# Kernel tuning notes

Hardware: AMD Instinct MI355X
Metric: run time of the kernel (lower is better)

## Reference

```python
import jax, jax.numpy as jnp
import numpy as np

B, T, I, E, H = 512, 1024, 32, 32, 256  # batch, seq, input, time-enc, hidden


def setup_inputs() -> dict:
    key = jax.random.key(0)
    ks = jax.random.split(key, 10)
    s = 0.05
    return {
        "X": jax.random.normal(ks[0], (B, T, I), dtype=jnp.float32),
        "encoded_timestamps": jax.random.normal(ks[1], (B, T, E), dtype=jnp.float32),
        "mask": jax.random.randint(ks[2], (B, T), 0, 2).astype(bool),
        # GRU layer 0: input = I + E
        "w_ih0": jax.random.normal(ks[3], (3 * H, I + E), dtype=jnp.float32) * s,
        "w_hh0": jax.random.normal(ks[4], (3 * H, H), dtype=jnp.float32) * s,
        "b_ih0": jnp.zeros((3 * H,), jnp.float32),
        "b_hh0": jnp.zeros((3 * H,), jnp.float32),
        # GRU layer 1: input = H
        "w_ih1": jax.random.normal(ks[5], (3 * H, H), dtype=jnp.float32) * s,
        "w_hh1": jax.random.normal(ks[6], (3 * H, H), dtype=jnp.float32) * s,
        "b_ih1": jnp.zeros((3 * H,), jnp.float32),
        "b_hh1": jnp.zeros((3 * H,), jnp.float32),
        # readout Linear(H -> I)
        "w_out": jax.random.normal(ks[7], (I, H), dtype=jnp.float32) * s,
        "b_out": jnp.zeros((I,), jnp.float32),
    }


def _gru_cell(x, h, w_ih, w_hh, b_ih, b_hh):
    # torch GRU cell semantics (gate order r, z, n)
    gi = x @ w_ih.T + b_ih
    gh = h @ w_hh.T + b_hh
    i_r, i_z, i_n = jnp.split(gi, 3, axis=-1)
    h_r, h_z, h_n = jnp.split(gh, 3, axis=-1)
    r = jax.nn.sigmoid(i_r + h_r)
    z = jax.nn.sigmoid(i_z + h_z)
    n = jnp.tanh(i_n + r * h_n)
    return (1.0 - z) * n + z * h


def reference(X, encoded_timestamps, mask,
              w_ih0, w_hh0, b_ih0, b_hh0,
              w_ih1, w_hh1, b_ih1, b_hh1,
              w_out, b_out):
    b, t, _ = X.shape
    hdim = w_hh0.shape[1]
    tm1 = t - 1

    def step(carry, xs):
        h0, h1, y = carry
        x_t, e_t, m_t, first = xs          # x_t [B,I], e_t [B,E], m_t [B], first scalar bool
        keep = m_t | first
        inp = jnp.concatenate([jnp.where(keep[:, None], x_t, y), e_t], axis=-1)
        h0 = _gru_cell(inp, h0, w_ih0, w_hh0, b_ih0, b_hh0)
        h1 = _gru_cell(h0, h1, w_ih1, w_hh1, b_ih1, b_hh1)
        y = h1 @ w_out.T + b_out
        return (h0, h1, y), y

    init = (jnp.zeros((b, hdim), X.dtype),
            jnp.zeros((b, hdim), X.dtype),
            jnp.zeros((b, X.shape[2]), X.dtype))
    xs = (jnp.swapaxes(X[:, :tm1], 0, 1),
          jnp.swapaxes(encoded_timestamps[:, 1:], 0, 1),
          jnp.swapaxes(mask[:, :tm1], 0, 1),
          jnp.arange(tm1) == 0)
    (h0, h1, _), outs = jax.lax.scan(step, init, xs)
    output_sequence = jnp.swapaxes(outs, 0, 1)  # [B, T-1, I]
    return output_sequence, h1  # h1 == h_t[-1]
```

## Files before the change

kernel.cpp:

```cpp
#include <hip/hip_runtime.h>
#include <stdint.h>
#include <stddef.h>

typedef unsigned short u16;
typedef unsigned int u32;
typedef unsigned long long u64;
typedef __attribute__((ext_vector_type(8))) short short8;
typedef __attribute__((ext_vector_type(4))) float f32x4;
typedef __attribute__((ext_vector_type(2))) float f32x2;

#define B_    512
#define T_    1024
#define TM1_  1023
#define I_    32
#define E_    32
#define H_    256
#define GSZ   16
#define NGRP  16
#define NTH   512
#define HBUF  (B_ * H_)
#define OUTY_STRIDE (TM1_ * I_)
#define OUTH_BASE ((size_t)B_ * TM1_ * I_)
#define FLAG_STRIDE 16

__device__ __forceinline__ u16 f2bf(float f) {
  union { float f; unsigned int i; } c;
  c.f = f;
  unsigned int x = c.i;
  x += 0x7FFFu + ((x >> 16) & 1u);
  return (u16)(x >> 16);
}
__device__ __forceinline__ short8 ld8bf(const float* p) {
  short8 rv;
#pragma unroll
  for (int j = 0; j < 8; ++j) rv[j] = (short)f2bf(p[j]);
  return rv;
}
__device__ __forceinline__ float sigm(float x) { return 1.f / (1.f + __expf(-x)); }
__device__ __forceinline__ float tanh_fast(float x) {
  x = fminf(15.f, fmaxf(-15.f, x));
  float e = __expf(2.f * x);
  return (e - 1.f) / (e + 1.f);
}
__device__ __forceinline__ u64 ldq_cp(const u64* p) { return *(volatile const u64*)p; }
__device__ __forceinline__ void stw_cp(u32* p, u32 v) { *(volatile u32*)p = v; }

__global__ __launch_bounds__(NTH, 2)
void arrnn_persistent(
    const float* __restrict__ X, const float* __restrict__ ENC, const int* __restrict__ MASK,
    const float* __restrict__ wih0, const float* __restrict__ whh0,
    const float* __restrict__ bih0, const float* __restrict__ bhh0,
    const float* __restrict__ wih1, const float* __restrict__ whh1,
    const float* __restrict__ bih1, const float* __restrict__ bhh1,
    const float* __restrict__ wout, const float* __restrict__ bout,
    float* __restrict__ out, u16* __restrict__ h0g, u16* __restrict__ h1g,
    int* __restrict__ flags)
{
  __shared__ __align__(16) u16 sH0buf[32 * 264];
  __shared__ __align__(16) u16 sH1buf[32 * 264];
  __shared__ __align__(16) u16 sXE[32 * 72];
  __shared__ float sGates[4 * 32 * 20];
  __shared__ float sH0loc[512];
  __shared__ float sH1loc[512];
  __shared__ float sY[32 * 36];
  __shared__ int   sMk[32];

  const int tid  = threadIdx.x;
  const int w    = tid >> 6;
  const int lane = tid & 63;
  const int quad = lane >> 4;
  const int l15  = lane & 15;
  const int g    = blockIdx.x >> 4;
  const int r    = blockIdx.x & 15;
  const int hs   = r << 4;
  const int row0 = g << 5;
  const int mt   = w & 1;
  const int gt   = w >> 1;
  const int crow = tid >> 4;
  const int cdim = tid & 15;

  short8 zero8 = {0, 0, 0, 0, 0, 0, 0, 0};

  const int grow = ((gt == 1) ? 256 : (gt >= 2 ? 512 : 0)) + hs + l15;

  short8 wfA[10];
#pragma unroll
  for (int kk = 0; kk < 10; ++kk) {
    const int k = kk * 32 + quad * 8;
    const float* p;
    bool v;
    if (gt <= 1)      { v = true;     p = (k < 64) ? (wih0 + grow * 64 + k)
                                                   : (whh0 + grow * 256 + (k - 64)); }
    else if (gt == 2) { v = (kk < 2); p = wih0 + grow * 64 + (v ? k : 0); }
    else              { v = (kk < 8); p = whh0 + grow * 256 + (v ? k : 0); }
    wfA[kk] = v ? ld8bf(p) : zero8;
  }

  short8 wfB[16];
#pragma unroll
  for (int kk = 0; kk < 16; ++kk) {
    const int k = kk * 32 + quad * 8;
    const float* p;
    bool v;
    if (gt <= 1)      { v = true;     p = (k < 256) ? (wih1 + grow * 256 + k)
                                                    : (whh1 + grow * 256 + (k - 256)); }
    else if (gt == 2) { v = (kk < 8); p = wih1 + grow * 256 + (v ? k : 0); }
    else              { v = (kk < 8); p = whh1 + grow * 256 + (v ? k : 0); }
    wfB[kk] = v ? ld8bf(p) : zero8;
  }

  const int yout = ((w >> 1) & 1) * 16 + l15;
  short8 wfY[8];
  if (w < 4) {
#pragma unroll
    for (int kk = 0; kk < 8; ++kk)
      wfY[kk] = ld8bf(wout + yout * 256 + kk * 32 + quad * 8);
  } else {
#pragma unroll
    for (int kk = 0; kk < 8; ++kk) wfY[kk] = zero8;
  }
  const float boutv = (w < 4) ? bout[yout] : 0.f;

  const int bd = hs + cdim;
  const float b0r  = bih0[bd]       + bhh0[bd];
  const float b0z  = bih0[256 + bd] + bhh0[256 + bd];
  const float b0ni = bih0[512 + bd];
  const float b0nh = bhh0[512 + bd];
  const float b1r  = bih1[bd]       + bhh1[bd];
  const float b1z  = bih1[256 + bd] + bhh1[256 + bd];
  const float b1ni = bih1[512 + bd];
  const float b1nh = bhh1[512 + bd];

  for (int i = tid; i < 4224; i += NTH) {
    ((u32*)sH0buf)[i] = 0u;
    ((u32*)sH1buf)[i] = 0u;
  }
  sH0loc[tid] = 0.f;
  sH1loc[tid] = 0.f;
  __syncthreads();

  const u64* h0q = (const u64*)h0g;
  const u64* h1q = (const u64*)h1g;
  u32* h0u = (u32*)h0g;
  u32* h1u = (u32*)h1g;

  int* fH0g  = flags + g * GSZ * FLAG_STRIDE;
  int* fH1g  = flags + NGRP * GSZ * FLAG_STRIDE + g * GSZ * FLAG_STRIDE;
  int* fH0own = fH0g + r * FLAG_STRIDE;
  int* fH1own = fH1g + r * FLAG_STRIDE;
  int alive = 1;

#define WAIT_FLAGS(basep, tgt)                                                   \
  do {                                                                           \
    int ok = 1;                                                                  \
    if (alive && lane < GSZ) {                                                   \
      const int* fp = (basep) + lane * FLAG_STRIDE;                              \
      int it = 0;                                                                \
      while (__hip_atomic_load(fp, __ATOMIC_RELAXED,                             \
                               __HIP_MEMORY_SCOPE_SYSTEM) < (tgt)) {             \
        __builtin_amdgcn_s_sleep(1);                                             \
        if (++it > (1 << 16)) { ok = 0; break; }                                 \
      }                                                                          \
    }                                                                            \
    if (__ballot(ok == 0) != 0ull) alive = 0;                                    \
  } while (0)

#define POST_FLAG(fp, val)                                                       \
  do {                                                                           \
    if (tid == 0) {                                                              \
      __builtin_amdgcn_s_waitcnt(0);                                             \
      __hip_atomic_store((fp), (val), __ATOMIC_RELAXED,                          \
                         __HIP_MEMORY_SCOPE_SYSTEM);                             \
    }                                                                            \
  } while (0)

  const int b = row0 + crow;
  const int arow = mt * 16 + l15;

  for (int t = 0; t < 1024; ++t) {
    const int par = t & 1;

    int mk = 1;
    if (t < 1023) {
      f32x2 xld = *(const f32x2*)(X   + ((size_t)b * T_ + t)     * I_ + 2 * cdim);
      f32x2 eld = *(const f32x2*)(ENC + ((size_t)b * T_ + t + 1) * E_ + 2 * cdim);
      if (t > 0) mk = (MASK[b * T_ + t] != 0);
      u16* A = sXE + crow * 72;
      const int c2 = 2 * cdim;
      if (mk) { A[c2] = f2bf(xld.x); A[c2 + 1] = f2bf(xld.y); }
      A[32 + c2] = f2bf(eld.x); A[32 + c2 + 1] = f2bf(eld.y);
      if (cdim == 0) sMk[crow] = mk;
    }

    f32x4 accA = {0.f, 0.f, 0.f, 0.f};
    if (t < 1023) {
      if (gt <= 1) {
        const u16* ah = sH0buf + arow * 264 + quad * 8;
#pragma unroll
        for (int kk = 2; kk < 10; ++kk) {
          short8 af = *(const short8*)(ah + (kk - 2) * 32);
          accA = __builtin_amdgcn_mfma_f32_16x16x32_bf16(af, wfA[kk], accA, 0, 0, 0);
        }
      } else if (gt == 3) {
        const u16* ah = sH0buf + arow * 264 + quad * 8;
#pragma unroll
        for (int kk = 0; kk < 8; ++kk) {
          short8 af = *(const short8*)(ah + kk * 32);
          accA = __builtin_amdgcn_mfma_f32_16x16x32_bf16(af, wfA[kk], accA, 0, 0, 0);
        }
      }
    }

    if (t > 0) {
      if (w == 0) WAIT_FLAGS(fH1g, t);
      __syncthreads();
      const u64* hq = h1q + (size_t)par * 32768 + (size_t)b * 64 + cdim * 4;
      u64 q0 = ldq_cp(hq), q1 = ldq_cp(hq + 1), q2 = ldq_cp(hq + 2), q3 = ldq_cp(hq + 3);
      union { u64 q[2]; short8 s; } u0, u1;
      u0.q[0] = q0; u0.q[1] = q1; u1.q[0] = q2; u1.q[1] = q3;
      *(short8*)(sH1buf + crow * 264 + cdim * 16)     = u0.s;
      *(short8*)(sH1buf + crow * 264 + cdim * 16 + 8) = u1.s;
    }
    __syncthreads();

    if (t > 0 && w < 4) {
      const u16* ap = sH1buf + (mt * 16 + l15) * 264 + quad * 8;
      f32x4 acc = {0.f, 0.f, 0.f, 0.f};
#pragma unroll
      for (int kk = 0; kk < 8; ++kk) {
        short8 af = *(const short8*)(ap + kk * 32);
        acc = __builtin_amdgcn_mfma_f32_16x16x32_bf16(af, wfY[kk], acc, 0, 0, 0);
      }
#pragma unroll
      for (int rg = 0; rg < 4; ++rg) {
        const int row = mt * 16 + quad * 4 + rg;
        const float yv = acc[rg] + boutv;
        sY[row * 36 + yout] = yv;
        if (t < 1023 && !sMk[row]) sXE[row * 72 + yout] = f2bf(yv);
      }
    }
    __syncthreads();

    if (t > 0 && tid < 64) {
      const int lr = r * 2 + (tid >> 5);
      const int lc = tid & 31;
      out[(size_t)(row0 + lr) * OUTY_STRIDE + (size_t)(t - 1) * I_ + lc] =
          sY[lr * 36 + lc];
    }
    if (t == 1023) break;

    if (gt <= 2) {
      const u16* axe = sXE + arow * 72 + quad * 8;
#pragma unroll
      for (int kk = 0; kk < 2; ++kk) {
        short8 af = *(const short8*)(axe + kk * 32);
        accA = __builtin_amdgcn_mfma_f32_16x16x32_bf16(af, wfA[kk], accA, 0, 0, 0);
      }
    }
#pragma unroll
    for (int rg = 0; rg < 4; ++rg)
      sGates[(gt * 32 + mt * 16 + quad * 4 + rg) * 20 + l15] = accA[rg];
    __syncthreads();

    {
      const float gr = sGates[(0 * 32 + crow) * 20 + cdim] + b0r;
      const float gz = sGates[(1 * 32 + crow) * 20 + cdim] + b0z;
      const float gi = sGates[(2 * 32 + crow) * 20 + cdim] + b0ni;
      const float gh = sGates[(3 * 32 + crow) * 20 + cdim] + b0nh;
      const float rr = sigm(gr);
      const float zz = sigm(gz);
      const float nn = tanh_fast(gi + rr * gh);
      const float hv = (1.f - zz) * nn + zz * sH0loc[tid];
      sH0loc[tid] = hv;
      const float hp = __shfl_xor(hv, 1, 64);
      if (!(tid & 1)) {
        u32 pk = (u32)f2bf(hv) | ((u32)f2bf(hp) << 16);
        stw_cp(h0u + (size_t)(par ^ 1) * 65536 + (size_t)b * 128 + ((hs + cdim) >> 1), pk);
      }
    }
    __syncthreads();
    POST_FLAG(fH0own, t + 1);

    f32x4 accB = {0.f, 0.f, 0.f, 0.f};
    if (gt <= 1) {
      const u16* a1 = sH1buf + arow * 264 + quad * 8;
#pragma unroll
      for (int kk = 0; kk < 8; ++kk) {
        short8 af = *(const short8*)(a1 + kk * 32);
        accB = __builtin_amdgcn_mfma_f32_16x16x32_bf16(af, wfB[kk + 8], accB, 0, 0, 0);
      }
    } else if (gt == 3) {
      const u16* a1 = sH1buf + arow * 264 + quad * 8;
#pragma unroll
      for (int kk = 0; kk < 8; ++kk) {
        short8 af = *(const short8*)(a1 + kk * 32);
        accB = __builtin_amdgcn_mfma_f32_16x16x32_bf16(af, wfB[kk], accB, 0, 0, 0);
      }
    }

    if (w == 0) WAIT_FLAGS(fH0g, t + 1);
    __syncthreads();
    {
      const u64* hq = h0q + (size_t)(par ^ 1) * 32768 + (size_t)b * 64 + cdim * 4;
      u64 q0 = ldq_cp(hq), q1 = ldq_cp(hq + 1), q2 = ldq_cp(hq + 2), q3 = ldq_cp(hq + 3);
      union { u64 q[2]; short8 s; } u0, u1;
      u0.q[0] = q0; u0.q[1] = q1; u1.q[0] = q2; u1.q[1] = q3;
      *(short8*)(sH0buf + crow * 264 + cdim * 16)     = u0.s;
      *(short8*)(sH0buf + crow * 264 + cdim * 16 + 8) = u1.s;
    }
    __syncthreads();

    if (gt <= 2) {
      const u16* a0 = sH0buf + arow * 264 + quad * 8;
#pragma unroll
      for (int kk = 0; kk < 8; ++kk) {
        short8 af = *(const short8*)(a0 + kk * 32);
        accB = __builtin_amdgcn_mfma_f32_16x16x32_bf16(af, wfB[kk], accB, 0, 0, 0);
      }
    }
#pragma unroll
    for (int rg = 0; rg < 4; ++rg)
      sGates[(gt * 32 + mt * 16 + quad * 4 + rg) * 20 + l15] = accB[rg];
    __syncthreads();

    {
      const float gr = sGates[(0 * 32 + crow) * 20 + cdim] + b1r;
      const float gz = sGates[(1 * 32 + crow) * 20 + cdim] + b1z;
      const float gi = sGates[(2 * 32 + crow) * 20 + cdim] + b1ni;
      const float gh = sGates[(3 * 32 + crow) * 20 + cdim] + b1nh;
      const float rr = sigm(gr);
      const float zz = sigm(gz);
      const float nn = tanh_fast(gi + rr * gh);
      const float hv = (1.f - zz) * nn + zz * sH1loc[tid];
      sH1loc[tid] = hv;
      const float hp = __shfl_xor(hv, 1, 64);
      if (!(tid & 1)) {
        u32 pk = (u32)f2bf(hv) | ((u32)f2bf(hp) << 16);
        stw_cp(h1u + (size_t)(par ^ 1) * 65536 + (size_t)b * 128 + ((hs + cdim) >> 1), pk);
      }
    }
    __syncthreads();
    POST_FLAG(fH1own, t + 1);
  }

  out[OUTH_BASE + (size_t)b * H_ + hs + cdim] = sH1loc[tid];
#undef WAIT_FLAGS
#undef POST_FLAG
}

extern "C" void kernel_launch(void* const* d_in, const int* in_sizes, int n_in,
                              void* d_out, int out_size, void* d_ws, size_t ws_size,
                              hipStream_t stream) {
  (void)in_sizes; (void)n_in; (void)out_size; (void)ws_size;
  const float* X    = (const float*)d_in[0];
  const float* ENC  = (const float*)d_in[1];
  const int*   MASK = (const int*)d_in[2];
  const float* wih0 = (const float*)d_in[3];
  const float* whh0 = (const float*)d_in[4];
  const float* bih0 = (const float*)d_in[5];
  const float* bhh0 = (const float*)d_in[6];
  const float* wih1 = (const float*)d_in[7];
  const float* whh1 = (const float*)d_in[8];
  const float* bih1 = (const float*)d_in[9];
  const float* bhh1 = (const float*)d_in[10];
  const float* wout = (const float*)d_in[11];
  const float* bout = (const float*)d_in[12];
  float* out = (float*)d_out;

  char* ws = (char*)d_ws;
  u16* h0g = (u16*)ws;
  u16* h1g = (u16*)(ws + 2 * (size_t)HBUF * 2);
  int* flags = (int*)(ws + 4 * (size_t)HBUF * 2);

  hipMemsetAsync(flags, 0, 2 * NGRP * GSZ * FLAG_STRIDE * sizeof(int), stream);
  arrnn_persistent<<<dim3(NGRP * GSZ), dim3(NTH), 0, stream>>>(
      X, ENC, MASK, wih0, whh0, bih0, bhh0, wih1, whh1, bih1, bhh1,
      wout, bout, out, h0g, h1g, flags);
}
```

Measured before the change: 6.313 ms.

## Replace flag barriers with tagged mailbox words and regroup into 8-block groups

Hidden-state exchange between blocks now uses a mailbox in which each 32-bit word carries a bf16 value and the step tag. Consumers spin directly on the data words instead of waiting on separate per-block flags, which removes the flag store/load round trip and some block-wide barriers. Groups change from 16 blocks of 32 rows to 8 blocks of 16 rows with a 32-wide hidden slice per block, so fewer peers take part in each group exchange. In exchange, mailbox traffic doubles because each value uses 32 bits, and every thread now spins on global memory.

Result: faster. 5.383 ms (-14.7%).

```diff
diff --git a/kernel.cpp b/kernel.cpp
--- a/kernel.cpp
+++ b/kernel.cpp
@@ -15,13 +15,12 @@
 #define I_    32
 #define E_    32
 #define H_    256
-#define GSZ   16
-#define NGRP  16
+#define GSZ   8
+#define NGRP  32
 #define NTH   512
-#define HBUF  (B_ * H_)
+#define MBOX_PAR (B_ * H_)
 #define OUTY_STRIDE (TM1_ * I_)
 #define OUTH_BASE ((size_t)B_ * TM1_ * I_)
-#define FLAG_STRIDE 16
 
 __device__ __forceinline__ u16 f2bf(float f) {
   union { float f; unsigned int i; } c;
@@ -53,35 +52,35 @@
     const float* __restrict__ wih1, const float* __restrict__ whh1,
     const float* __restrict__ bih1, const float* __restrict__ bhh1,
     const float* __restrict__ wout, const float* __restrict__ bout,
-    float* __restrict__ out, u16* __restrict__ h0g, u16* __restrict__ h1g,
-    int* __restrict__ flags)
+    float* __restrict__ out, u32* __restrict__ h0m, u32* __restrict__ h1m)
 {
-  __shared__ __align__(16) u16 sH0buf[32 * 264];
-  __shared__ __align__(16) u16 sH1buf[32 * 264];
-  __shared__ __align__(16) u16 sXE[32 * 72];
-  __shared__ float sGates[4 * 32 * 20];
+  __shared__ __align__(16) u16 sH0buf[16 * 264];
+  __shared__ __align__(16) u16 sH1buf[16 * 264];
+  __shared__ __align__(16) u16 sXE[16 * 72];
+  __shared__ float sGates[8 * 16 * 20];
   __shared__ float sH0loc[512];
   __shared__ float sH1loc[512];
-  __shared__ float sY[32 * 36];
-  __shared__ int   sMk[32];
+  __shared__ float sY[16 * 36];
+  __shared__ int   sMk[16];
 
   const int tid  = threadIdx.x;
   const int w    = tid >> 6;
   const int lane = tid & 63;
   const int quad = lane >> 4;
   const int l15  = lane & 15;
-  const int g    = blockIdx.x >> 4;
-  const int r    = blockIdx.x & 15;
-  const int hs   = r << 4;
-  const int row0 = g << 5;
-  const int mt   = w & 1;
+  const int g    = blockIdx.x >> 3;
+  const int r    = blockIdx.x & 7;
+  const int hs   = r << 5;
+  const int row0 = g << 4;
   const int gt   = w >> 1;
-  const int crow = tid >> 4;
-  const int cdim = tid & 15;
+  const int nt   = w & 1;
+  const int crow = tid >> 5;
+  const int c32  = tid & 31;
 
   short8 zero8 = {0, 0, 0, 0, 0, 0, 0, 0};
 
-  const int grow = ((gt == 1) ? 256 : (gt >= 2 ? 512 : 0)) + hs + l15;
+  const int gateofs = (gt == 1) ? 256 : (gt >= 2 ? 512 : 0);
+  const int grow = gateofs + hs + (nt << 4) + l15;
 
   short8 wfA[10];
 #pragma unroll
@@ -109,19 +108,19 @@
     wfB[kk] = v ? ld8bf(p) : zero8;
   }
 
-  const int yout = ((w >> 1) & 1) * 16 + l15;
+  const int ycol = (w << 4) + l15;
   short8 wfY[8];
-  if (w < 4) {
+  if (w < 2) {
 #pragma unroll
     for (int kk = 0; kk < 8; ++kk)
-      wfY[kk] = ld8bf(wout + yout * 256 + kk * 32 + quad * 8);
+      wfY[kk] = ld8bf(wout + ycol * 256 + kk * 32 + quad * 8);
   } else {
 #pragma unroll
     for (int kk = 0; kk < 8; ++kk) wfY[kk] = zero8;
   }
-  const float boutv = (w < 4) ? bout[yout] : 0.f;
-
-  const int bd = hs + cdim;
+  const float boutv = (w < 2) ? bout[ycol] : 0.f;
+
+  const int bd = hs + c32;
   const float b0r  = bih0[bd]       + bhh0[bd];
   const float b0z  = bih0[256 + bd] + bhh0[256 + bd];
   const float b0ni = bih0[512 + bd];
@@ -131,7 +130,7 @@
   const float b1ni = bih1[512 + bd];
   const float b1nh = bhh1[512 + bd];
 
-  for (int i = tid; i < 4224; i += NTH) {
+  for (int i = tid; i < 2112; i += NTH) {
     ((u32*)sH0buf)[i] = 0u;
     ((u32*)sH1buf)[i] = 0u;
   }
@@ -139,213 +138,170 @@
   sH1loc[tid] = 0.f;
   __syncthreads();
 
-  const u64* h0q = (const u64*)h0g;
-  const u64* h1q = (const u64*)h1g;
-  u32* h0u = (u32*)h0g;
-  u32* h1u = (u32*)h1g;
-
-  int* fH0g  = flags + g * GSZ * FLAG_STRIDE;
-  int* fH1g  = flags + NGRP * GSZ * FLAG_STRIDE + g * GSZ * FLAG_STRIDE;
-  int* fH0own = fH0g + r * FLAG_STRIDE;
-  int* fH1own = fH1g + r * FLAG_STRIDE;
   int alive = 1;
-
-#define WAIT_FLAGS(basep, tgt)                                                   \
+  const int b = row0 + crow;
+
+#define SPIN_STAGE(mboxu32, expTag, dstbuf)                                      \
   do {                                                                           \
-    int ok = 1;                                                                  \
-    if (alive && lane < GSZ) {                                                   \
-      const int* fp = (basep) + lane * FLAG_STRIDE;                              \
-      int it = 0;                                                                \
-      while (__hip_atomic_load(fp, __ATOMIC_RELAXED,                             \
-                               __HIP_MEMORY_SCOPE_SYSTEM) < (tgt)) {             \
-        __builtin_amdgcn_s_sleep(1);                                             \
-        if (++it > (1 << 16)) { ok = 0; break; }                                 \
-      }                                                                          \
+    const u64* qp = (const u64*)(mboxu32) + (size_t)b * 128 + c32 * 4;           \
+    const u64 tagp = (u64)(u32)(expTag) | ((u64)(u32)(expTag) << 32);            \
+    u64 q0, q1, q2, q3;                                                          \
+    int it = 0;                                                                  \
+    for (;;) {                                                                   \
+      q0 = ldq_cp(qp); q1 = ldq_cp(qp + 1); q2 = ldq_cp(qp + 2); q3 = ldq_cp(qp + 3); \
+      u64 dd = ((q0 ^ tagp) | (q1 ^ tagp) | (q2 ^ tagp) | (q3 ^ tagp))           \
+               & 0x0000FFFF0000FFFFull;                                          \
+      if (dd == 0 || !alive) break;                                              \
+      if (++it > (1 << 16)) { alive = 0; break; }                                \
     }                                                                            \
-    if (__ballot(ok == 0) != 0ull) alive = 0;                                    \
+    short8 sv;                                                                   \
+    sv[0] = (short)(u16)(q0 >> 16); sv[1] = (short)(u16)(q0 >> 48);              \
+    sv[2] = (short)(u16)(q1 >> 16); sv[3] = (short)(u16)(q1 >> 48);              \
+    sv[4] = (short)(u16)(q2 >> 16); sv[5] = (short)(u16)(q2 >> 48);              \
+    sv[6] = (short)(u16)(q3 >> 16); sv[7] = (short)(u16)(q3 >> 48);              \
+    *(short8*)((dstbuf) + crow * 264 + c32 * 8) = sv;                            \
   } while (0)
-
-#define POST_FLAG(fp, val)                                                       \
-  do {                                                                           \
-    if (tid == 0) {                                                              \
-      __builtin_amdgcn_s_waitcnt(0);                                             \
-      __hip_atomic_store((fp), (val), __ATOMIC_RELAXED,                          \
-                         __HIP_MEMORY_SCOPE_SYSTEM);                             \
-    }                                                                            \
-  } while (0)
-
-  const int b = row0 + crow;
-  const int arow = mt * 16 + l15;
 
   for (int t = 0; t < 1024; ++t) {
     const int par = t & 1;
 
     int mk = 1;
     if (t < 1023) {
-      f32x2 xld = *(const f32x2*)(X   + ((size_t)b * T_ + t)     * I_ + 2 * cdim);
-      f32x2 eld = *(const f32x2*)(ENC + ((size_t)b * T_ + t + 1) * E_ + 2 * cdim);
-      if (t > 0) mk = (MASK[b * T_ + t] != 0);
-      u16* A = sXE + crow * 72;
-      const int c2 = 2 * cdim;
-      if (mk) { A[c2] = f2bf(xld.x); A[c2 + 1] = f2bf(xld.y); }
-      A[32 + c2] = f2bf(eld.x); A[32 + c2 + 1] = f2bf(eld.y);
-      if (cdim == 0) sMk[crow] = mk;
+      if (c32 < 16) {
+        if (t > 0) mk = (MASK[b * T_ + t] != 0);
+        f32x2 xld = *(const f32x2*)(X + ((size_t)b * T_ + t) * I_ + 2 * c32);
+        if (mk) { sXE[crow * 72 + 2 * c32] = f2bf(xld.x);
+                  sXE[crow * 72 + 2 * c32 + 1] = f2bf(xld.y); }
+        if (c32 == 0) sMk[crow] = mk;
+      } else {
+        const int c2 = c32 - 16;
+        f32x2 eld = *(const f32x2*)(ENC + ((size_t)b * T_ + t + 1) * E_ + 2 * c2);
+        sXE[crow * 72 + 32 + 2 * c2] = f2bf(eld.x);
+        sXE[crow * 72 + 32 + 2 * c2 + 1] = f2bf(eld.y);
+      }
     }
 
     f32x4 accA = {0.f, 0.f, 0.f, 0.f};
     if (t < 1023) {
+      const u16* ah = sH0buf + l15 * 264 + quad * 8;
       if (gt <= 1) {
-        const u16* ah = sH0buf + arow * 264 + quad * 8;
-#pragma unroll
-        for (int kk = 2; kk < 10; ++kk) {
-          short8 af = *(const short8*)(ah + (kk - 2) * 32);
-          accA = __builtin_amdgcn_mfma_f32_16x16x32_bf16(af, wfA[kk], accA, 0, 0, 0);
-        }
+#pragma unroll
+        for (int kk = 2; kk < 10; ++kk)
+          accA = __builtin_amdgcn_mfma_f32_16x16x32_bf16(
+              *(const short8*)(ah + (kk - 2) * 32), wfA[kk], accA, 0, 0, 0);
       } else if (gt == 3) {
-        const u16* ah = sH0buf + arow * 264 + quad * 8;
-#pragma unroll
-        for (int kk = 0; kk < 8; ++kk) {
-          short8 af = *(const short8*)(ah + kk * 32);
-          accA = __builtin_amdgcn_mfma_f32_16x16x32_bf16(af, wfA[kk], accA, 0, 0, 0);
-        }
+#pragma unroll
+        for (int kk = 0; kk < 8; ++kk)
+          accA = __builtin_amdgcn_mfma_f32_16x16x32_bf16(
+              *(const short8*)(ah + kk * 32), wfA[kk], accA, 0, 0, 0);
       }
     }
 
+    if (t > 0) SPIN_STAGE(h1m + (size_t)par * MBOX_PAR, t, sH1buf);
+    __syncthreads();
+
+    if (t > 0 && w < 2) {
+      const u16* ap = sH1buf + l15 * 264 + quad * 8;
+      f32x4 acc = {0.f, 0.f, 0.f, 0.f};
+#pragma unroll
+      for (int kk = 0; kk < 8; ++kk)
+        acc = __builtin_amdgcn_mfma_f32_16x16x32_bf16(
+            *(const short8*)(ap + kk * 32), wfY[kk], acc, 0, 0, 0);
+#pragma unroll
+      for (int rg = 0; rg < 4; ++rg)
+        sY[(quad * 4 + rg) * 36 + ycol] = acc[rg] + boutv;
+    }
+    __syncthreads();
+
     if (t > 0) {
-      if (w == 0) WAIT_FLAGS(fH1g, t);
-      __syncthreads();
-      const u64* hq = h1q + (size_t)par * 32768 + (size_t)b * 64 + cdim * 4;
-      u64 q0 = ldq_cp(hq), q1 = ldq_cp(hq + 1), q2 = ldq_cp(hq + 2), q3 = ldq_cp(hq + 3);
-      union { u64 q[2]; short8 s; } u0, u1;
-      u0.q[0] = q0; u0.q[1] = q1; u1.q[0] = q2; u1.q[1] = q3;
-      *(short8*)(sH1buf + crow * 264 + cdim * 16)     = u0.s;
-      *(short8*)(sH1buf + crow * 264 + cdim * 16 + 8) = u1.s;
-    }
-    __syncthreads();
-
-    if (t > 0 && w < 4) {
-      const u16* ap = sH1buf + (mt * 16 + l15) * 264 + quad * 8;
-      f32x4 acc = {0.f, 0.f, 0.f, 0.f};
-#pragma unroll
-      for (int kk = 0; kk < 8; ++kk) {
-        short8 af = *(const short8*)(ap + kk * 32);
-        acc = __builtin_amdgcn_mfma_f32_16x16x32_bf16(af, wfY[kk], acc, 0, 0, 0);
+      if (tid < 64) {
+        const int lr = (r << 1) + (tid >> 5);
+        const int lc = tid & 31;
+        out[(size_t)(row0 + lr) * OUTY_STRIDE + (size_t)(t - 1) * I_ + lc] =
+            sY[lr * 36 + lc];
       }
-#pragma unroll
-      for (int rg = 0; rg < 4; ++rg) {
-        const int row = mt * 16 + quad * 4 + rg;
-        const float yv = acc[rg] + boutv;
-        sY[row * 36 + yout] = yv;
-        if (t < 1023 && !sMk[row]) sXE[row * 72 + yout] = f2bf(yv);
-      }
-    }
-    __syncthreads();
-
-    if (t > 0 && tid < 64) {
-      const int lr = r * 2 + (tid >> 5);
-      const int lc = tid & 31;
-      out[(size_t)(row0 + lr) * OUTY_STRIDE + (size_t)(t - 1) * I_ + lc] =
-          sY[lr * 36 + lc];
+      if (t < 1023 && !sMk[crow])
+        sXE[crow * 72 + c32] = f2bf(sY[crow * 36 + c32]);
     }
     if (t == 1023) break;
+    __syncthreads();
 
     if (gt <= 2) {
-      const u16* axe = sXE + arow * 72 + quad * 8;
-#pragma unroll
-      for (int kk = 0; kk < 2; ++kk) {
-        short8 af = *(const short8*)(axe + kk * 32);
-        accA = __builtin_amdgcn_mfma_f32_16x16x32_bf16(af, wfA[kk], accA, 0, 0, 0);
-      }
+      const u16* axe = sXE + l15 * 72 + quad * 8;
+#pragma unroll
+      for (int kk = 0; kk < 2; ++kk)
+        accA = __builtin_amdgcn_mfma_f32_16x16x32_bf16(
+            *(const short8*)(axe + kk * 32), wfA[kk], accA, 0, 0, 0);
     }
 #pragma unroll
     for (int rg = 0; rg < 4; ++rg)
-      sGates[(gt * 32 + mt * 16 + quad * 4 + rg) * 20 + l15] = accA[rg];
+      sGates[((gt << 1) | nt) * 320 + (quad * 4 + rg) * 20 + l15] = accA[rg];
     __syncthreads();
 
     {
-      const float gr = sGates[(0 * 32 + crow) * 20 + cdim] + b0r;
-      const float gz = sGates[(1 * 32 + crow) * 20 + cdim] + b0z;
-      const float gi = sGates[(2 * 32 + crow) * 20 + cdim] + b0ni;
-      const float gh = sGates[(3 * 32 + crow) * 20 + cdim] + b0nh;
+      const int ntc = c32 >> 4, cc = c32 & 15;
+      const float gr = sGates[((0 << 1) | ntc) * 320 + crow * 20 + cc] + b0r;
+      const float gz = sGates[((1 << 1) | ntc) * 320 + crow * 20 + cc] + b0z;
+      const float gi = sGates[((2 << 1) | ntc) * 320 + crow * 20 + cc] + b0ni;
+      const float gh = sGates[((3 << 1) | ntc) * 320 + crow * 20 + cc] + b0nh;
       const float rr = sigm(gr);
       const float zz = sigm(gz);
       const float nn = tanh_fast(gi + rr * gh);
       const float hv = (1.f - zz) * nn + zz * sH0loc[tid];
       sH0loc[tid] = hv;
-      const float hp = __shfl_xor(hv, 1, 64);
-      if (!(tid & 1)) {
-        u32 pk = (u32)f2bf(hv) | ((u32)f2bf(hp) << 16);
-        stw_cp(h0u + (size_t)(par ^ 1) * 65536 + (size_t)b * 128 + ((hs + cdim) >> 1), pk);
+      stw_cp(h0m + (size_t)(par ^ 1) * MBOX_PAR + (size_t)b * H_ + hs + c32,
+             ((u32)f2bf(hv) << 16) | (u32)(t + 1));
+    }
+
+    f32x4 accB = {0.f, 0.f, 0.f, 0.f};
+    {
+      const u16* a1 = sH1buf + l15 * 264 + quad * 8;
+      if (gt <= 1) {
+#pragma unroll
+        for (int kk = 0; kk < 8; ++kk)
+          accB = __builtin_amdgcn_mfma_f32_16x16x32_bf16(
+              *(const short8*)(a1 + kk * 32), wfB[kk + 8], accB, 0, 0, 0);
+      } else if (gt == 3) {
+#pragma unroll
+        for (int kk = 0; kk < 8; ++kk)
+          accB = __builtin_amdgcn_mfma_f32_16x16x32_bf16(
+              *(const short8*)(a1 + kk * 32), wfB[kk], accB, 0, 0, 0);
       }
     }
-    __syncthreads();
-    POST_FLAG(fH0own, t + 1);
-
-    f32x4 accB = {0.f, 0.f, 0.f, 0.f};
-    if (gt <= 1) {
-      const u16* a1 = sH1buf + arow * 264 + quad * 8;
-#pragma unroll
-      for (int kk = 0; kk < 8; ++kk) {
-        short8 af = *(const short8*)(a1 + kk * 32);
-        accB = __builtin_amdgcn_mfma_f32_16x16x32_bf16(af, wfB[kk + 8], accB, 0, 0, 0);
-      }
-    } else if (gt == 3) {
-      const u16* a1 = sH1buf + arow * 264 + quad * 8;
-#pragma unroll
-      for (int kk = 0; kk < 8; ++kk) {
-        short8 af = *(const short8*)(a1 + kk * 32);
-        accB = __builtin_amdgcn_mfma_f32_16x16x32_bf16(af, wfB[kk], accB, 0, 0, 0);
-      }
-    }
-
-    if (w == 0) WAIT_FLAGS(fH0g, t + 1);
-    __syncthreads();
+
+    SPIN_STAGE(h0m + (size_t)(par ^ 1) * MBOX_PAR, t + 1, sH0buf);
+    __syncthreads();
+
+    if (gt <= 2) {
+      const u16* a0 = sH0buf + l15 * 264 + quad * 8;
+#pragma unroll
+      for (int kk = 0; kk < 8; ++kk)
+        accB = __builtin_amdgcn_mfma_f32_16x16x32_bf16(
+            *(const short8*)(a0 + kk * 32), wfB[kk], accB, 0, 0, 0);
+    }
+#pragma unroll
+    for (int rg = 0; rg < 4; ++rg)
+      sGates[((gt << 1) | nt) * 320 + (quad * 4 + rg) * 20 + l15] = accB[rg];
+    __syncthreads();
+
     {
-      const u64* hq = h0q + (size_t)(par ^ 1) * 32768 + (size_t)b * 64 + cdim * 4;
-      u64 q0 = ldq_cp(hq), q1 = ldq_cp(hq + 1), q2 = ldq_cp(hq + 2), q3 = ldq_cp(hq + 3);
-      union { u64 q[2]; short8 s; } u0, u1;
-      u0.q[0] = q0; u0.q[1] = q1; u1.q[0] = q2; u1.q[1] = q3;
-      *(short8*)(sH0buf + crow * 264 + cdim * 16)     = u0.s;
-      *(short8*)(sH0buf + crow * 264 + cdim * 16 + 8) = u1.s;
-    }
-    __syncthreads();
-
-    if (gt <= 2) {
-      const u16* a0 = sH0buf + arow * 264 + quad * 8;
-#pragma unroll
-      for (int kk = 0; kk < 8; ++kk) {
-        short8 af = *(const short8*)(a0 + kk * 32);
-        accB = __builtin_amdgcn_mfma_f32_16x16x32_bf16(af, wfB[kk], accB, 0, 0, 0);
-      }
-    }
-#pragma unroll
-    for (int rg = 0; rg < 4; ++rg)
-      sGates[(gt * 32 + mt * 16 + quad * 4 + rg) * 20 + l15] = accB[rg];
-    __syncthreads();
-
-    {
-      const float gr = sGates[(0 * 32 + crow) * 20 + cdim] + b1r;
-      const float gz = sGates[(1 * 32 + crow) * 20 + cdim] + b1z;
-      const float gi = sGates[(2 * 32 + crow) * 20 + cdim] + b1ni;
-      const float gh = sGates[(3 * 32 + crow) * 20 + cdim] + b1nh;
+      const int ntc = c32 >> 4, cc = c32 & 15;
+      const float gr = sGates[((0 << 1) | ntc) * 320 + crow * 20 + cc] + b1r;
+      const float gz = sGates[((1 << 1) | ntc) * 320 + crow * 20 + cc] + b1z;
+      const float gi = sGates[((2 << 1) | ntc) * 320 + crow * 20 + cc] + b1ni;
+      const float gh = sGates[((3 << 1) | ntc) * 320 + crow * 20 + cc] + b1nh;
       const float rr = sigm(gr);
       const float zz = sigm(gz);
       const float nn = tanh_fast(gi + rr * gh);
       const float hv = (1.f - zz) * nn + zz * sH1loc[tid];
       sH1loc[tid] = hv;
-      const float hp = __shfl_xor(hv, 1, 64);
-      if (!(tid & 1)) {
-        u32 pk = (u32)f2bf(hv) | ((u32)f2bf(hp) << 16);
-        stw_cp(h1u + (size_t)(par ^ 1) * 65536 + (size_t)b * 128 + ((hs + cdim) >> 1), pk);
-      }
-    }
-    __syncthreads();
-    POST_FLAG(fH1own, t + 1);
-  }
-
-  out[OUTH_BASE + (size_t)b * H_ + hs + cdim] = sH1loc[tid];
-#undef WAIT_FLAGS
-#undef POST_FLAG
+      stw_cp(h1m + (size_t)(par ^ 1) * MBOX_PAR + (size_t)b * H_ + hs + c32,
+             ((u32)f2bf(hv) << 16) | (u32)(t + 1));
+    }
+  }
+
+  out[OUTH_BASE + (size_t)b * H_ + hs + c32] = sH1loc[tid];
+#undef SPIN_STAGE
 }
 
 extern "C" void kernel_launch(void* const* d_in, const int* in_sizes, int n_in,
@@ -367,13 +323,11 @@
   const float* bout = (const float*)d_in[12];
   float* out = (float*)d_out;
 
-  char* ws = (char*)d_ws;
-  u16* h0g = (u16*)ws;
-  u16* h1g = (u16*)(ws + 2 * (size_t)HBUF * 2);
-  int* flags = (int*)(ws + 4 * (size_t)HBUF * 2);
-
-  hipMemsetAsync(flags, 0, 2 * NGRP * GSZ * FLAG_STRIDE * sizeof(int), stream);
+  u32* h0m = (u32*)d_ws;
+  u32* h1m = h0m + 2 * (size_t)MBOX_PAR;
+
+  hipMemsetAsync(h0m, 0, 4 * (size_t)MBOX_PAR * sizeof(u32), stream);
   arrnn_persistent<<<dim3(NGRP * GSZ), dim3(NTH), 0, stream>>>(
       X, ENC, MASK, wih0, whh0, bih0, bhh0, wih1, whh1, bih1, bhh1,
-      wout, bout, out, h0g, h1g, flags);
-}
+      wout, bout, out, h0m, h1m);
+}
```
